# Kernel tuning notes

Measured on AMD Instinct MI355X. Metric: run time of the kernel, lower is better.

## Reference

```python
import jax, jax.numpy as jnp
import numpy as np

N, NH, D, REP, C, SUB = 512, 32, 1024, 1024, 16, 64
GAMA, EPS, LN_EPS = 0.9, 1e-10, 1e-5
IMG_H, IMG_W = 800, 1280


def spatial_enc(b1, b2, h, w):
    # pocket.ops.compute_spatial_encodings: 18 handcrafted pair features + their logs -> 36
    c1x = (b1[:, 0] + b1[:, 2]) * 0.5; c1y = (b1[:, 1] + b1[:, 3]) * 0.5
    c2x = (b2[:, 0] + b2[:, 2]) * 0.5; c2y = (b2[:, 1] + b2[:, 3]) * 0.5
    b1w = b1[:, 2] - b1[:, 0]; b1h = b1[:, 3] - b1[:, 1]
    b2w = b2[:, 2] - b2[:, 0]; b2h = b2[:, 3] - b2[:, 1]
    dx = jnp.abs(c2x - c1x) / (b1w + EPS)
    dy = jnp.abs(c2y - c1y) / (b1h + EPS)
    ltx = jnp.maximum(b1[:, 0], b2[:, 0]); lty = jnp.maximum(b1[:, 1], b2[:, 1])
    rbx = jnp.minimum(b1[:, 2], b2[:, 2]); rby = jnp.minimum(b1[:, 3], b2[:, 3])
    inter = jnp.clip(rbx - ltx, 0.0) * jnp.clip(rby - lty, 0.0)
    a1 = b1w * b1h; a2 = b2w * b2h
    iou = inter / (a1 + a2 - inter)
    f = jnp.stack([
        c1x / w, c1y / h, c2x / w, c2y / h,
        b1w / w, b1h / h, b2w / w, b2h / h,
        a1 / (h * w), a2 / (h * w), a2 / (a1 + EPS),
        b1w / (b1h + EPS), b2w / (b2h + EPS), iou,
        (c2x > c1x) * dx, (c2x < c1x) * dx,
        (c2y > c1y) * dy, (c2y < c1y) * dy,
    ], axis=1)
    return jnp.concatenate([f, jnp.log(f + EPS)], axis=1)


def mbf(a, s, w1, b1, w2, b2, w3, b3):
    # relu(sum_c fc3_c(relu(fc1_c(a) * fc2_c(s)))) with branches batched over c
    u1 = jnp.einsum('pd,cdk->cpk', a, w1) + b1[:, None, :]
    u2 = jnp.einsum('ps,csk->cpk', s, w2) + b2[:, None, :]
    hdn = jax.nn.relu(u1 * u2)  # [C,P,SUB]
    out = jnp.einsum('cpk,cko->po', hdn, w3) + b3.sum(0)
    return jax.nn.relu(out)


def ln(x, g, b):
    m = x.mean(-1, keepdims=True)
    v = ((x - m) ** 2).mean(-1, keepdims=True)
    return (x - m) / jnp.sqrt(v + LN_EPS) * g + b


def setup_inputs():
    key = jax.random.key(0)
    ks = jax.random.split(key, 16)
    labels = jnp.where(jnp.arange(N) < NH, 0, 1).astype(jnp.int32)  # first NH nodes are humans
    node = jax.random.normal(ks[0], (N, D), jnp.float32)
    cx = jax.random.uniform(ks[1], (N,)) * (IMG_W * 0.5)
    cy = jax.random.uniform(ks[2], (N,)) * (IMG_H * 0.5)
    bw = jax.random.uniform(ks[3], (N,)) * (IMG_W * 0.3) + 8.0
    bh = jax.random.uniform(ks[4], (N,)) * (IMG_H * 0.3) + 8.0
    coords = jnp.stack([cx, cy, cx + bw, cy + bh], axis=1)
    p = lambda k, shp: jax.random.normal(k, shp, jnp.float32) * 0.02
    return dict(
        labels=labels, node=node, coords=coords, image_h=IMG_H, image_w=IMG_W,
        sp_w1=p(ks[5], (36, 128)), sp_b1=jnp.zeros(128),
        sp_w2=p(ks[6], (128, 256)), sp_b2=jnp.zeros(256),
        sp_w3=p(ks[7], (256, 1024)), sp_b3=jnp.zeros(1024),
        att_w1=p(ks[8], (C, 2 * D, SUB)), att_b1=jnp.zeros((C, SUB)),
        att_w2=p(ks[9], (C, 1024, SUB)), att_b2=jnp.zeros((C, SUB)),
        att_w3=p(ks[10], (C, SUB, REP)), att_b3=jnp.zeros((C, REP)),
        adj_w=p(ks[11], (REP,)), adj_b=jnp.zeros(()),
        lnh_g=jnp.ones(D), lnh_b=jnp.zeros(D),
        lno_g=jnp.ones(D), lno_b=jnp.zeros(D),
    )


def reference(labels, node, coords, image_h, image_w,
              sp_w1, sp_b1, sp_w2, sp_b2, sp_w3, sp_b3,
              att_w1, att_b1, att_w2, att_b2, att_w3, att_b3,
              adj_w, adj_b, lnh_g, lnh_b, lno_g, lno_b):
    n = node.shape[0]
    n_h = int((np.asarray(labels) == 0).sum())
    xi = np.repeat(np.arange(n_h), n)  # human index per pair
    yj = np.tile(np.arange(n), n_h)    # node index per pair
    keep = np.nonzero(xi != yj)[0]
    x = jnp.asarray(xi); y = jnp.asarray(yj)
    x_keep = jnp.asarray(xi[keep]); y_keep = jnp.asarray(yj[keep])

    f = spatial_enc(coords[x], coords[y], float(image_h), float(image_w))  # [P,36]
    sp = jax.nn.relu(f @ sp_w1 + sp_b1)
    sp = jax.nn.relu(sp @ sp_w2 + sp_b2)
    sp = jax.nn.relu(sp @ sp_w3 + sp_b3)  # [P,1024]

    human_node = node[:n_h]
    adjacency = None
    for _ in range(2):  # num_iter
        a = jnp.concatenate([human_node[x], node[y]], axis=1)  # [P,2D]
        weight = mbf(a, sp, att_w1, att_b1, att_w2, att_b2, att_w3, att_b3)  # [P,REP]
        adjacency = jax.nn.relu(weight @ adj_w + adj_b).reshape(n_h, n)
        hn_msg = adjacency @ node          # einsum('yx,xa->ya', adj, node)
        nd_msg = adjacency.T @ human_node  # einsum('yx,xa->ya', adj.T, human)
        node = ln(node * GAMA + (1.0 - GAMA) * nd_msg, lno_g, lno_b)
        human_node = ln(human_node * GAMA + (1.0 - GAMA) * hn_msg, lnh_g, lnh_b)

    return (human_node[x_keep], node[y_keep], adjacency[x_keep, y_keep], x_keep, y_keep)
```

## Files before the change

kernel.cpp:

```cpp
#include <hip/hip_runtime.h>
#include <hip/hip_bf16.h>


typedef __attribute__((ext_vector_type(4))) float  f32x4;
typedef __attribute__((ext_vector_type(8))) __bf16 bf16x8;
typedef __attribute__((ext_vector_type(4))) __bf16 bf16x4;

#define FEPS 1e-10f
#define LNEPS 1e-5f
#define GAMA_F 0.9f

__device__ __forceinline__ void gload16(const void* g, void* l) {
  __builtin_amdgcn_global_load_lds(
      (const __attribute__((address_space(1))) void*)g,
      (__attribute__((address_space(3))) void*)l, 16, 0, 0);
}

__global__ void prep_all(const float* __restrict__ w1, const float* __restrict__ w2,
                         const float* __restrict__ w3, const float* __restrict__ spw3,
                         __bf16* __restrict__ W1at, __bf16* __restrict__ W1bt,
                         __bf16* __restrict__ W2t, __bf16* __restrict__ W3t,
                         __bf16* __restrict__ SpW3t) {
  __shared__ float tile[64][65];
  const int b = blockIdx.x, t = threadIdx.x;
  const int tc = t & 63, tr = t >> 6;
  if (b < 256) {
    const int c = b >> 4, d0 = (b & 15) << 6;
    #pragma unroll
    for (int pass = 0; pass < 2; ++pass) {
      const float* src = w1 + (size_t)c * 131072 + (size_t)(d0 + pass * 1024) * 64;
      __bf16* dst = pass ? W1bt : W1at;
      if (pass) __syncthreads();
      #pragma unroll
      for (int q = 0; q < 16; ++q) {
        int dd = q * 4 + tr;
        tile[dd][tc] = src[dd * 64 + tc];
      }
      __syncthreads();
      #pragma unroll
      for (int q = 0; q < 16; ++q) {
        int kk = q * 4 + tr;
        dst[(size_t)(c * 64 + kk) * 1024 + d0 + tc] = (__bf16)tile[tc][kk];
      }
    }
  } else if (b < 512) {
    const int bb = b - 256, c = bb >> 4, s0 = (bb & 15) << 6;
    const float* src = w2 + (size_t)c * 65536 + (size_t)s0 * 64;
    #pragma unroll
    for (int q = 0; q < 16; ++q) {
      int ss = q * 4 + tr;
      tile[ss][tc] = src[ss * 64 + tc];
    }
    __syncthreads();
    #pragma unroll
    for (int q = 0; q < 16; ++q) {
      int kk = q * 4 + tr;
      W2t[(size_t)(c * 64 + kk) * 1024 + s0 + tc] = (__bf16)tile[tc][kk];
    }
  } else if (b < 768) {
    const int bb = b - 512, c = bb >> 4, o0 = (bb & 15) << 6;
    const float* src = w3 + (size_t)c * 65536;
    #pragma unroll
    for (int q = 0; q < 16; ++q) {
      int kk = q * 4 + tr;
      tile[kk][tc] = src[kk * 1024 + o0 + tc];
    }
    __syncthreads();
    #pragma unroll
    for (int q = 0; q < 16; ++q) {
      int oo = q * 4 + tr;
      W3t[(size_t)(o0 + oo) * 1024 + c * 64 + tc] = (__bf16)tile[tc][oo];
    }
  } else {
    const int bb = b - 768, o0 = (bb >> 2) << 6, k0 = (bb & 3) << 6;
    #pragma unroll
    for (int q = 0; q < 16; ++q) {
      int kk = q * 4 + tr;
      tile[kk][tc] = spw3[(size_t)(k0 + kk) * 1024 + o0 + tc];
    }
    __syncthreads();
    #pragma unroll
    for (int q = 0; q < 16; ++q) {
      int oo = q * 4 + tr;
      SpW3t[(size_t)(o0 + oo) * 256 + k0 + tc] = (__bf16)tile[tc][oo];
    }
  }
}

__global__ void prep_sp2(const float* __restrict__ w1, const float* __restrict__ w2,
                         const float* __restrict__ b3,
                         __bf16* __restrict__ W1t, __bf16* __restrict__ W2t,
                         float* __restrict__ b3s) {
  int gid = blockIdx.x * 256 + threadIdx.x;
  if (gid < 8192) {
    int n = gid >> 6, k = gid & 63;
    W1t[gid] = (k < 36) ? (__bf16)w1[k * 128 + n] : (__bf16)0.f;
  }
  {
    int n = gid >> 7, k = gid & 127;
    W2t[gid] = (__bf16)w2[k * 256 + n];
  }
  if (gid < 1024) {
    float s = 0.f;
    for (int cc = 0; cc < 16; ++cc) s += b3[cc * 1024 + gid];
    b3s[gid] = s;
  }
}

__global__ void init_nodes(const float* __restrict__ node_in, float* __restrict__ node_f,
                           __bf16* __restrict__ node_b, float* __restrict__ hn_f,
                           __bf16* __restrict__ hn_b) {
  int gid = blockIdx.x * 256 + threadIdx.x;
  float v = node_in[gid];
  node_f[gid] = v;
  node_b[gid] = (__bf16)v;
  if (gid < 32 * 1024) { hn_f[gid] = v; hn_b[gid] = (__bf16)v; }
}

__device__ __forceinline__ float read_dim(const void* p) {
  int iv = *(const int*)p;
  if (iv > 0 && iv < (1 << 20)) return (float)iv;
  return *(const float*)p;
}

__global__ void spatial_k(const float* __restrict__ coords, const void* __restrict__ imh,
                          const void* __restrict__ imw, __bf16* __restrict__ f36) {
  int p = blockIdx.x * 256 + threadIdx.x;
  int i = p >> 9, j = p & 511;
  float H = read_dim(imh), W = read_dim(imw);
  f32x4 b1 = ((const f32x4*)coords)[i];
  f32x4 b2 = ((const f32x4*)coords)[j];
  float c1x = (b1[0] + b1[2]) * 0.5f, c1y = (b1[1] + b1[3]) * 0.5f;
  float c2x = (b2[0] + b2[2]) * 0.5f, c2y = (b2[1] + b2[3]) * 0.5f;
  float b1w = b1[2] - b1[0], b1h = b1[3] - b1[1];
  float b2w = b2[2] - b2[0], b2h = b2[3] - b2[1];
  float dx = fabsf(c2x - c1x) / (b1w + FEPS);
  float dy = fabsf(c2y - c1y) / (b1h + FEPS);
  float ltx = fmaxf(b1[0], b2[0]), lty = fmaxf(b1[1], b2[1]);
  float rbx = fminf(b1[2], b2[2]), rby = fminf(b1[3], b2[3]);
  float inter = fmaxf(rbx - ltx, 0.f) * fmaxf(rby - lty, 0.f);
  float a1 = b1w * b1h, a2 = b2w * b2h;
  float iou = inter / (a1 + a2 - inter);
  float f[18];
  f[0] = c1x / W;  f[1] = c1y / H;  f[2] = c2x / W;  f[3] = c2y / H;
  f[4] = b1w / W;  f[5] = b1h / H;  f[6] = b2w / W;  f[7] = b2h / H;
  f[8] = a1 / (H * W); f[9] = a2 / (H * W); f[10] = a2 / (a1 + FEPS);
  f[11] = b1w / (b1h + FEPS); f[12] = b2w / (b2h + FEPS); f[13] = iou;
  f[14] = (c2x > c1x) ? dx : 0.f; f[15] = (c2x < c1x) ? dx : 0.f;
  f[16] = (c2y > c1y) ? dy : 0.f; f[17] = (c2y < c1y) ? dy : 0.f;
  __bf16 o[64];
  #pragma unroll
  for (int q = 0; q < 18; ++q) { o[q] = (__bf16)f[q]; o[18 + q] = (__bf16)logf(f[q] + FEPS); }
  #pragma unroll
  for (int q = 36; q < 64; ++q) o[q] = (__bf16)0.f;
  bf16x8* dst = (bf16x8*)(f36 + (size_t)p * 64);
  #pragma unroll
  for (int q = 0; q < 8; ++q) dst[q] = *(bf16x8*)&o[q * 8];
}

template <int EPI>
__global__ __launch_bounds__(256)
void gemm_bt(const __bf16* __restrict__ A, const __bf16* __restrict__ Bt,
             const float* __restrict__ bias, void* __restrict__ C,
             int M, int N, int K,
             const float* __restrict__ adjw = nullptr,
             float* __restrict__ adjpre = nullptr) {
  __shared__ __align__(16) __bf16 As[128 * 64];
  __shared__ __align__(16) __bf16 Bs[128 * 64];
  const int t = threadIdx.x;
  const int lane = t & 63, wv = t >> 6;
  const int wr = wv >> 1, wc = wv & 1;
  const int lr = lane & 15, lg = lane >> 4;
  const int lrow = lane >> 3, lcol = (lane & 7) << 3;
  const int m0 = blockIdx.x * 128, n0 = blockIdx.y * 128;

  f32x4 acc[4][4] = {};
  const int nkt = K >> 6;
  for (int kt = 0; kt < nkt; ++kt) {
    const int k0 = kt << 6;
    #pragma unroll
    for (int it = 0; it < 4; ++it) {
      const int rbase = wv * 32 + it * 8;
      gload16(A + (size_t)(m0 + rbase + lrow) * K + k0 + lcol, &As[rbase * 64]);
      gload16(Bt + (size_t)(n0 + rbase + lrow) * K + k0 + lcol, &Bs[rbase * 64]);
    }
    __syncthreads();
    #pragma unroll
    for (int ks = 0; ks < 2; ++ks) {
      bf16x8 af[4], bfr[4];
      #pragma unroll
      for (int mi = 0; mi < 4; ++mi)
        af[mi] = *(const bf16x8*)&As[(wr * 64 + mi * 16 + lr) * 64 + ks * 32 + lg * 8];
      #pragma unroll
      for (int ni = 0; ni < 4; ++ni)
        bfr[ni] = *(const bf16x8*)&Bs[(wc * 64 + ni * 16 + lr) * 64 + ks * 32 + lg * 8];
      #pragma unroll
      for (int mi = 0; mi < 4; ++mi)
        #pragma unroll
        for (int ni = 0; ni < 4; ++ni)
          acc[mi][ni] = __builtin_amdgcn_mfma_f32_16x16x32_bf16(af[mi], bfr[ni], acc[mi][ni], 0, 0, 0);
    }
    __syncthreads();
  }

  if constexpr (EPI == 4) {
    float b3v[4], awv[4];
    #pragma unroll
    for (int ni = 0; ni < 4; ++ni) {
      int Cc = n0 + wc * 64 + ni * 16 + lr;
      b3v[ni] = bias[Cc];
      awv[ni] = adjw[Cc];
    }
    #pragma unroll
    for (int mi = 0; mi < 4; ++mi) {
      #pragma unroll
      for (int r = 0; r < 4; ++r) {
        float s = 0.f;
        #pragma unroll
        for (int ni = 0; ni < 4; ++ni)
          s += fmaxf(acc[mi][ni][r] + b3v[ni], 0.f) * awv[ni];
        s += __shfl_xor(s, 1);
        s += __shfl_xor(s, 2);
        s += __shfl_xor(s, 4);
        s += __shfl_xor(s, 8);
        if (lr == 0)
          atomicAdd(&adjpre[m0 + wr * 64 + mi * 16 + lg * 4 + r], s);
      }
    }
  } else {
    #pragma unroll
    for (int mi = 0; mi < 4; ++mi) {
      #pragma unroll
      for (int r = 0; r < 4; ++r) {
        int R = m0 + wr * 64 + mi * 16 + lg * 4 + r;
        #pragma unroll
        for (int ni = 0; ni < 4; ++ni) {
          int Cc = n0 + wc * 64 + ni * 16 + lr;
          float v = acc[mi][ni][r];
          if constexpr (EPI == 0) {
            ((__bf16*)C)[(size_t)R * N + Cc] = (__bf16)fmaxf(v + bias[Cc], 0.f);
          } else if constexpr (EPI == 1) {
            ((__bf16*)C)[(size_t)R * N + Cc] = (__bf16)(v + bias[Cc]);
          } else if constexpr (EPI == 2) {
            ((float*)C)[(size_t)R * N + Cc] = v + bias[Cc];
          } else {
            ((float*)C)[(size_t)R * N + Cc] = v;
          }
        }
      }
    }
  }
}

__global__ __launch_bounds__(256)
void gemm_u1(const __bf16* __restrict__ hn_b, const __bf16* __restrict__ node_b,
             const __bf16* __restrict__ W1at, const __bf16* __restrict__ W1bt,
             const float* __restrict__ b1, float* __restrict__ H1, float* __restrict__ N1) {
  __shared__ __align__(16) __bf16 As[32 * 64];
  __shared__ __align__(16) __bf16 Bs[128 * 64];
  const int t = threadIdx.x;
  const int lane = t & 63, wv = t >> 6;
  const int wr = wv >> 1, wc = wv & 1;
  const int lr = lane & 15, lg = lane >> 4;
  const int lrow = lane >> 3, lcol = (lane & 7) << 3;
  const bool isH = (blockIdx.x == 0);
  const __bf16* Ap = isH ? hn_b : node_b + (size_t)(blockIdx.x - 1) * 32 * 1024;
  const __bf16* Bp = isH ? W1at : W1bt;
  const int n0 = blockIdx.y * 128;

  f32x4 acc[4] = {};
  for (int kt = 0; kt < 16; ++kt) {
    const int k0 = kt << 6;
    gload16(Ap + (size_t)(wv * 8 + lrow) * 1024 + k0 + lcol, &As[(wv * 8) * 64]);
    #pragma unroll
    for (int it = 0; it < 4; ++it) {
      const int rbase = wv * 32 + it * 8;
      gload16(Bp + (size_t)(n0 + rbase + lrow) * 1024 + k0 + lcol, &Bs[rbase * 64]);
    }
    __syncthreads();
    #pragma unroll
    for (int ks = 0; ks < 2; ++ks) {
      bf16x8 af = *(const bf16x8*)&As[(wr * 16 + lr) * 64 + ks * 32 + lg * 8];
      #pragma unroll
      for (int ni = 0; ni < 4; ++ni) {
        bf16x8 bfr = *(const bf16x8*)&Bs[(wc * 64 + ni * 16 + lr) * 64 + ks * 32 + lg * 8];
        acc[ni] = __builtin_amdgcn_mfma_f32_16x16x32_bf16(af, bfr, acc[ni], 0, 0, 0);
      }
    }
    __syncthreads();
  }
  #pragma unroll
  for (int ni = 0; ni < 4; ++ni) {
    #pragma unroll
    for (int r = 0; r < 4; ++r) {
      int R = wr * 16 + lg * 4 + r;
      int Cc = n0 + wc * 64 + ni * 16 + lr;
      float v = acc[ni][r];
      if (isH) H1[(size_t)R * 1024 + Cc] = v + b1[Cc];
      else     N1[((size_t)(blockIdx.x - 1) * 32 + R) * 1024 + Cc] = v;
    }
  }
}

__global__ void build_hdn(const __bf16* __restrict__ u2, const float* __restrict__ H1,
                          const float* __restrict__ N1, __bf16* __restrict__ hdn) {
  int gid = blockIdx.x * 256 + threadIdx.x;
  int p = gid >> 7, c8 = (gid & 127) << 3;
  int i = p >> 9, j = p & 511;
  bf16x8 u = *(const bf16x8*)(u2 + (size_t)p * 1024 + c8);
  const float* hp = H1 + (size_t)i * 1024 + c8;
  const float* np = N1 + (size_t)j * 1024 + c8;
  f32x4 h0 = *(const f32x4*)hp, h1 = *(const f32x4*)(hp + 4);
  f32x4 n0 = *(const f32x4*)np, n1 = *(const f32x4*)(np + 4);
  bf16x8 o;
  #pragma unroll
  for (int e = 0; e < 4; ++e) {
    o[e]     = (__bf16)fmaxf((h0[e] + n0[e]) * (float)u[e], 0.f);
    o[4 + e] = (__bf16)fmaxf((h1[e] + n1[e]) * (float)u[4 + e], 0.f);
  }
  *(bf16x8*)(hdn + (size_t)p * 1024 + c8) = o;
}

__global__ void msg_k(const float* __restrict__ adjpre, const float* __restrict__ adjb,
                      const float* __restrict__ node, const float* __restrict__ hn,
                      float* __restrict__ hn_msg, float* __restrict__ nd_msg) {
  int row = blockIdx.x, t = threadIdx.x;
  float ab = adjb[0];
  if (row < 32) {
    f32x4 acc = {0.f, 0.f, 0.f, 0.f};
    for (int j = 0; j < 512; ++j)
      acc += fmaxf(adjpre[row * 512 + j] + ab, 0.f) * ((const f32x4*)node)[j * 256 + t];
    ((f32x4*)hn_msg)[row * 256 + t] = acc;
  } else {
    int j = row - 32;
    f32x4 acc = {0.f, 0.f, 0.f, 0.f};
    for (int i = 0; i < 32; ++i)
      acc += fmaxf(adjpre[i * 512 + j] + ab, 0.f) * ((const f32x4*)hn)[i * 256 + t];
    ((f32x4*)nd_msg)[j * 256 + t] = acc;
  }
}

__global__ void ln_k(float* __restrict__ node_f, float* __restrict__ hn_f,
                     const float* __restrict__ nd_msg, const float* __restrict__ hn_msg,
                     const float* __restrict__ lno_g, const float* __restrict__ lno_b,
                     const float* __restrict__ lnh_g, const float* __restrict__ lnh_b,
                     __bf16* __restrict__ node_bb, __bf16* __restrict__ hn_bb) {
  __shared__ float sbuf[4];
  int row = blockIdx.x, t = threadIdx.x;
  bool isN = row < 512;
  int r = isN ? row : row - 512;
  float* X = (isN ? node_f : hn_f) + (size_t)r * 1024;
  const float* Mg = (isN ? nd_msg : hn_msg) + (size_t)r * 1024;
  const float* g = isN ? lno_g : lnh_g;
  const float* bb = isN ? lno_b : lnh_b;
  __bf16* Xb = (isN ? node_bb : hn_bb) + (size_t)r * 1024;

  f32x4 x = ((const f32x4*)X)[t];
  f32x4 m = ((const f32x4*)Mg)[t];
  f32x4 y;
  #pragma unroll
  for (int e = 0; e < 4; ++e) y[e] = x[e] * GAMA_F + (1.0f - GAMA_F) * m[e];
  float s = y[0] + y[1] + y[2] + y[3];
  #pragma unroll
  for (int mm = 32; mm >= 1; mm >>= 1) s += __shfl_xor(s, mm);
  if ((t & 63) == 0) sbuf[t >> 6] = s;
  __syncthreads();
  float mean = (sbuf[0] + sbuf[1] + sbuf[2] + sbuf[3]) * (1.0f / 1024.0f);
  __syncthreads();
  f32x4 d;
  #pragma unroll
  for (int e = 0; e < 4; ++e) d[e] = y[e] - mean;
  float sq = d[0] * d[0] + d[1] * d[1] + d[2] * d[2] + d[3] * d[3];
  #pragma unroll
  for (int mm = 32; mm >= 1; mm >>= 1) sq += __shfl_xor(sq, mm);
  if ((t & 63) == 0) sbuf[t >> 6] = sq;
  __syncthreads();
  float var = (sbuf[0] + sbuf[1] + sbuf[2] + sbuf[3]) * (1.0f / 1024.0f);
  float inv = rsqrtf(var + LNEPS);
  f32x4 gg = ((const f32x4*)g)[t];
  f32x4 bv = ((const f32x4*)bb)[t];
  f32x4 o;
  bf16x4 ob;
  #pragma unroll
  for (int e = 0; e < 4; ++e) { o[e] = d[e] * inv * gg[e] + bv[e]; ob[e] = (__bf16)o[e]; }
  ((f32x4*)X)[t] = o;
  *(bf16x4*)(Xb + t * 4) = ob;
}

__global__ void gather_k(const float* __restrict__ hn, const float* __restrict__ node,
                         const float* __restrict__ adjpre, const float* __restrict__ adjb,
                         float* __restrict__ out) {
  int p = blockIdx.x, t = threadIdx.x;
  int i = p >> 9, j = p & 511;
  if (i == j) return;
  int m = p - (p + 512) / 513;
  float* out0 = out;
  float* out1 = out + (size_t)16352 * 1024;
  float* out2 = out1 + (size_t)16352 * 1024;
  ((f32x4*)out0)[(size_t)m * 256 + t] = ((const f32x4*)hn)[i * 256 + t];
  ((f32x4*)out1)[(size_t)m * 256 + t] = ((const f32x4*)node)[j * 256 + t];
  if (t == 0) {
    out2[m] = fmaxf(adjpre[p] + adjb[0], 0.f);
    out2[16352 + m] = (float)i;
    out2[2 * 16352 + m] = (float)j;
  }
}

extern "C" void kernel_launch(void* const* d_in, const int* in_sizes, int n_in,
                              void* d_out, int out_size, void* d_ws, size_t ws_size,
                              hipStream_t stream) {
  const float* node_in = (const float*)d_in[1];
  const float* coords  = (const float*)d_in[2];
  const void*  imh     = d_in[3];
  const void*  imw     = d_in[4];
  const float* sp_w1 = (const float*)d_in[5];
  const float* sp_b1 = (const float*)d_in[6];
  const float* sp_w2 = (const float*)d_in[7];
  const float* sp_b2 = (const float*)d_in[8];
  const float* sp_w3 = (const float*)d_in[9];
  const float* sp_b3 = (const float*)d_in[10];
  const float* att_w1 = (const float*)d_in[11];
  const float* att_b1 = (const float*)d_in[12];
  const float* att_w2 = (const float*)d_in[13];
  const float* att_b2 = (const float*)d_in[14];
  const float* att_w3 = (const float*)d_in[15];
  const float* att_b3 = (const float*)d_in[16];
  const float* adj_w  = (const float*)d_in[17];
  const float* adj_b  = (const float*)d_in[18];
  const float* lnh_g  = (const float*)d_in[19];
  const float* lnh_b  = (const float*)d_in[20];
  const float* lno_g  = (const float*)d_in[21];
  const float* lno_b  = (const float*)d_in[22];

  char* w = (char*)d_ws;
  size_t off = 0;
  auto alloc = [&](size_t bytes) -> char* {
    char* p = w + off;
    off += (bytes + 255) & ~(size_t)255;
    return p;
  };
  __bf16* W1at  = (__bf16*)alloc((size_t)1024 * 1024 * 2);
  __bf16* W1bt  = (__bf16*)alloc((size_t)1024 * 1024 * 2);
  __bf16* W2t   = (__bf16*)alloc((size_t)1024 * 1024 * 2);
  __bf16* W3t   = (__bf16*)alloc((size_t)1024 * 1024 * 2);
  __bf16* SpW1t = (__bf16*)alloc(128 * 64 * 2);
  __bf16* SpW2t = (__bf16*)alloc(256 * 128 * 2);
  __bf16* SpW3t = (__bf16*)alloc(1024 * 256 * 2);
  float*  b3s   = (float*)alloc(1024 * 4);
  __bf16* f36   = (__bf16*)alloc((size_t)16384 * 64 * 2);
  __bf16* sp1   = (__bf16*)alloc((size_t)16384 * 128 * 2);
  __bf16* sp2   = (__bf16*)alloc((size_t)16384 * 256 * 2);
  __bf16* spb   = (__bf16*)alloc((size_t)16384 * 1024 * 2);
  __bf16* u2    = (__bf16*)alloc((size_t)16384 * 1024 * 2);
  float*  H1    = (float*)alloc((size_t)32 * 1024 * 4);
  float*  N1    = (float*)alloc((size_t)512 * 1024 * 4);
  float*  adjpre = (float*)alloc(16384 * 4);
  float*  node_f = (float*)alloc((size_t)512 * 1024 * 4);
  float*  hn_f   = (float*)alloc((size_t)32 * 1024 * 4);
  __bf16* node_b = (__bf16*)alloc((size_t)512 * 1024 * 2);
  __bf16* hn_b   = (__bf16*)alloc((size_t)32 * 1024 * 2);
  float*  hn_msgb = (float*)alloc((size_t)32 * 1024 * 4);
  float*  nd_msgb = (float*)alloc((size_t)512 * 1024 * 4);
  if (off > ws_size) return;

  prep_all<<<832, 256, 0, stream>>>(att_w1, att_w2, att_w3, sp_w3, W1at, W1bt, W2t, W3t, SpW3t);
  prep_sp2<<<128, 256, 0, stream>>>(sp_w1, sp_w2, att_b3, SpW1t, SpW2t, b3s);
  init_nodes<<<2048, 256, 0, stream>>>(node_in, node_f, node_b, hn_f, hn_b);
  spatial_k<<<64, 256, 0, stream>>>(coords, imh, imw, f36);

  gemm_bt<0><<<dim3(128, 1), 256, 0, stream>>>(f36, SpW1t, sp_b1, sp1, 16384, 128, 64);
  gemm_bt<0><<<dim3(128, 2), 256, 0, stream>>>(sp1, SpW2t, sp_b2, sp2, 16384, 256, 128);
  gemm_bt<0><<<dim3(128, 8), 256, 0, stream>>>(sp2, SpW3t, sp_b3, spb, 16384, 1024, 256);
  gemm_bt<1><<<dim3(128, 8), 256, 0, stream>>>(spb, W2t, att_b2, u2, 16384, 1024, 1024);

  __bf16* hdn = spb;
  for (int iter = 0; iter < 2; ++iter) {
    gemm_u1<<<dim3(17, 8), 256, 0, stream>>>(hn_b, node_b, W1at, W1bt, att_b1, H1, N1);
    build_hdn<<<8192, 256, 0, stream>>>(u2, H1, N1, hdn);
    hipMemsetAsync(adjpre, 0, 16384 * 4, stream);
    gemm_bt<4><<<dim3(128, 8), 256, 0, stream>>>(hdn, W3t, b3s, nullptr, 16384, 1024, 1024,
                                                 adj_w, adjpre);
    msg_k<<<544, 256, 0, stream>>>(adjpre, adj_b, node_f, hn_f, hn_msgb, nd_msgb);
    ln_k<<<544, 256, 0, stream>>>(node_f, hn_f, nd_msgb, hn_msgb,
                                  lno_g, lno_b, lnh_g, lnh_b, node_b, hn_b);
  }

  gather_k<<<16384, 256, 0, stream>>>(hn_f, node_f, adjpre, adj_b, (float*)d_out);
}
```

Measured before the change: 525.6 us.

## Fuse prep kernels, MLP head, hdn build into GEMM, and msg+LN

Merges the four prep kernels into one launch and fuses the first two spatial MLP layers into a single kernel that keeps the intermediate in LDS. build_hdn is folded into the A-operand load of the W3 GEMM, which now splits N into four 256-wide slices and writes per-slice partial sums instead of using atomics and a memset. msg_k and ln_k are merged, with ping-pong node buffers. The aim is fewer launches and no 32MB hdn round trip, at the cost of recomputing the hdn elementwise per column slice and uncoalesced loads of u2 and N1 in the GEMM.

Measured after the change: 598.2 us. 13.8% more time.

```diff
diff --git a/kernel.cpp b/kernel.cpp
--- a/kernel.cpp
+++ b/kernel.cpp
@@ -16,11 +16,27 @@
       (__attribute__((address_space(3))) void*)l, 16, 0, 0);
 }
 
-__global__ void prep_all(const float* __restrict__ w1, const float* __restrict__ w2,
-                         const float* __restrict__ w3, const float* __restrict__ spw3,
-                         __bf16* __restrict__ W1at, __bf16* __restrict__ W1bt,
-                         __bf16* __restrict__ W2t, __bf16* __restrict__ W3t,
-                         __bf16* __restrict__ SpW3t) {
+__device__ __forceinline__ float read_dim(const void* p) {
+  int iv = *(const int*)p;
+  if (iv > 0 && iv < (1 << 20)) return (float)iv;
+  return *(const float*)p;
+}
+
+__global__ void prep_mega(const float* __restrict__ w1, const float* __restrict__ w2,
+                          const float* __restrict__ w3, const float* __restrict__ spw3,
+                          const float* __restrict__ spw1, const float* __restrict__ spw2,
+                          const float* __restrict__ b3,
+                          const float* __restrict__ node_in,
+                          const float* __restrict__ coords,
+                          const void* __restrict__ imh, const void* __restrict__ imw,
+                          __bf16* __restrict__ W1at, __bf16* __restrict__ W1bt,
+                          __bf16* __restrict__ W2t, __bf16* __restrict__ W3t,
+                          __bf16* __restrict__ SpW3t,
+                          __bf16* __restrict__ SpW1t, __bf16* __restrict__ SpW2t,
+                          float* __restrict__ b3s,
+                          float* __restrict__ node_f, __bf16* __restrict__ node_b,
+                          float* __restrict__ hn_f, __bf16* __restrict__ hn_b,
+                          __bf16* __restrict__ f36) {
   __shared__ float tile[64][65];
   const int b = blockIdx.x, t = threadIdx.x;
   const int tc = t & 63, tr = t >> 6;
@@ -71,7 +87,7 @@
       int oo = q * 4 + tr;
       W3t[(size_t)(o0 + oo) * 1024 + c * 64 + tc] = (__bf16)tile[tc][oo];
     }
-  } else {
+  } else if (b < 832) {
     const int bb = b - 768, o0 = (bb >> 2) << 6, k0 = (bb & 3) << 6;
     #pragma unroll
     for (int q = 0; q < 16; ++q) {
@@ -84,87 +100,154 @@
       int oo = q * 4 + tr;
       SpW3t[(size_t)(o0 + oo) * 256 + k0 + tc] = (__bf16)tile[tc][oo];
     }
-  }
-}
-
-__global__ void prep_sp2(const float* __restrict__ w1, const float* __restrict__ w2,
-                         const float* __restrict__ b3,
-                         __bf16* __restrict__ W1t, __bf16* __restrict__ W2t,
-                         float* __restrict__ b3s) {
-  int gid = blockIdx.x * 256 + threadIdx.x;
-  if (gid < 8192) {
-    int n = gid >> 6, k = gid & 63;
-    W1t[gid] = (k < 36) ? (__bf16)w1[k * 128 + n] : (__bf16)0.f;
-  }
+  } else if (b < 960) {
+    int gid = (b - 832) * 256 + t;
+    if (gid < 8192) {
+      int n = gid >> 6, k = gid & 63;
+      SpW1t[gid] = (k < 36) ? (__bf16)spw1[k * 128 + n] : (__bf16)0.f;
+    }
+    {
+      int n = gid >> 7, k = gid & 127;
+      SpW2t[gid] = (__bf16)spw2[k * 256 + n];
+    }
+    if (gid < 1024) {
+      float s = 0.f;
+      for (int cc = 0; cc < 16; ++cc) s += b3[cc * 1024 + gid];
+      b3s[gid] = s;
+    }
+  } else if (b < 3008) {
+    int gid = (b - 960) * 256 + t;
+    float v = node_in[gid];
+    node_f[gid] = v;
+    node_b[gid] = (__bf16)v;
+    if (gid < 32 * 1024) { hn_f[gid] = v; hn_b[gid] = (__bf16)v; }
+  } else {
+    int p = (b - 3008) * 256 + t;
+    int i = p >> 9, j = p & 511;
+    float H = read_dim(imh), W = read_dim(imw);
+    f32x4 b1 = ((const f32x4*)coords)[i];
+    f32x4 b2 = ((const f32x4*)coords)[j];
+    float c1x = (b1[0] + b1[2]) * 0.5f, c1y = (b1[1] + b1[3]) * 0.5f;
+    float c2x = (b2[0] + b2[2]) * 0.5f, c2y = (b2[1] + b2[3]) * 0.5f;
+    float b1w = b1[2] - b1[0], b1h = b1[3] - b1[1];
+    float b2w = b2[2] - b2[0], b2h = b2[3] - b2[1];
+    float dx = fabsf(c2x - c1x) / (b1w + FEPS);
+    float dy = fabsf(c2y - c1y) / (b1h + FEPS);
+    float ltx = fmaxf(b1[0], b2[0]), lty = fmaxf(b1[1], b2[1]);
+    float rbx = fminf(b1[2], b2[2]), rby = fminf(b1[3], b2[3]);
+    float inter = fmaxf(rbx - ltx, 0.f) * fmaxf(rby - lty, 0.f);
+    float a1 = b1w * b1h, a2 = b2w * b2h;
+    float iou = inter / (a1 + a2 - inter);
+    float f[18];
+    f[0] = c1x / W;  f[1] = c1y / H;  f[2] = c2x / W;  f[3] = c2y / H;
+    f[4] = b1w / W;  f[5] = b1h / H;  f[6] = b2w / W;  f[7] = b2h / H;
+    f[8] = a1 / (H * W); f[9] = a2 / (H * W); f[10] = a2 / (a1 + FEPS);
+    f[11] = b1w / (b1h + FEPS); f[12] = b2w / (b2h + FEPS); f[13] = iou;
+    f[14] = (c2x > c1x) ? dx : 0.f; f[15] = (c2x < c1x) ? dx : 0.f;
+    f[16] = (c2y > c1y) ? dy : 0.f; f[17] = (c2y < c1y) ? dy : 0.f;
+    __bf16 o[64];
+    #pragma unroll
+    for (int q = 0; q < 18; ++q) { o[q] = (__bf16)f[q]; o[18 + q] = (__bf16)logf(f[q] + FEPS); }
+    #pragma unroll
+    for (int q = 36; q < 64; ++q) o[q] = (__bf16)0.f;
+    bf16x8* dst = (bf16x8*)(f36 + (size_t)p * 64);
+    #pragma unroll
+    for (int q = 0; q < 8; ++q) dst[q] = *(bf16x8*)&o[q * 8];
+  }
+}
+
+__global__ __launch_bounds__(256)
+void mlp_head(const __bf16* __restrict__ f36, const __bf16* __restrict__ SpW1t,
+              const __bf16* __restrict__ SpW2t, const float* __restrict__ b1,
+              const float* __restrict__ b2, __bf16* __restrict__ sp2out) {
+  __shared__ __align__(16) __bf16 Af[128 * 64];
+  __shared__ __align__(16) __bf16 W1s[128 * 64];
+  __shared__ __align__(16) __bf16 S1[128 * 128];
+  __shared__ __align__(16) __bf16 W2s[256 * 128];
+  const int t = threadIdx.x;
+  const int lane = t & 63, wv = t >> 6;
+  const int wr = wv >> 1, wc = wv & 1;
+  const int lr = lane & 15, lg = lane >> 4;
+  const int m0 = blockIdx.x * 128;
+
+  #pragma unroll
+  for (int cc = 0; cc < 4; ++cc)
+    gload16(f36 + (size_t)m0 * 64 + (wv * 4 + cc) * 512 + lane * 8, &Af[(wv * 4 + cc) * 512 + lane * 8]);
+  #pragma unroll
+  for (int cc = 0; cc < 4; ++cc)
+    gload16(SpW1t + (wv * 4 + cc) * 512 + lane * 8, &W1s[(wv * 4 + cc) * 512 + lane * 8]);
+  #pragma unroll
+  for (int cc = 0; cc < 16; ++cc)
+    gload16(SpW2t + (wv * 16 + cc) * 512 + lane * 8, &W2s[(wv * 16 + cc) * 512 + lane * 8]);
+  __syncthreads();
+
   {
-    int n = gid >> 7, k = gid & 127;
-    W2t[gid] = (__bf16)w2[k * 256 + n];
-  }
-  if (gid < 1024) {
-    float s = 0.f;
-    for (int cc = 0; cc < 16; ++cc) s += b3[cc * 1024 + gid];
-    b3s[gid] = s;
-  }
-}
-
-__global__ void init_nodes(const float* __restrict__ node_in, float* __restrict__ node_f,
-                           __bf16* __restrict__ node_b, float* __restrict__ hn_f,
-                           __bf16* __restrict__ hn_b) {
-  int gid = blockIdx.x * 256 + threadIdx.x;
-  float v = node_in[gid];
-  node_f[gid] = v;
-  node_b[gid] = (__bf16)v;
-  if (gid < 32 * 1024) { hn_f[gid] = v; hn_b[gid] = (__bf16)v; }
-}
-
-__device__ __forceinline__ float read_dim(const void* p) {
-  int iv = *(const int*)p;
-  if (iv > 0 && iv < (1 << 20)) return (float)iv;
-  return *(const float*)p;
-}
-
-__global__ void spatial_k(const float* __restrict__ coords, const void* __restrict__ imh,
-                          const void* __restrict__ imw, __bf16* __restrict__ f36) {
-  int p = blockIdx.x * 256 + threadIdx.x;
-  int i = p >> 9, j = p & 511;
-  float H = read_dim(imh), W = read_dim(imw);
-  f32x4 b1 = ((const f32x4*)coords)[i];
-  f32x4 b2 = ((const f32x4*)coords)[j];
-  float c1x = (b1[0] + b1[2]) * 0.5f, c1y = (b1[1] + b1[3]) * 0.5f;
-  float c2x = (b2[0] + b2[2]) * 0.5f, c2y = (b2[1] + b2[3]) * 0.5f;
-  float b1w = b1[2] - b1[0], b1h = b1[3] - b1[1];
-  float b2w = b2[2] - b2[0], b2h = b2[3] - b2[1];
-  float dx = fabsf(c2x - c1x) / (b1w + FEPS);
-  float dy = fabsf(c2y - c1y) / (b1h + FEPS);
-  float ltx = fmaxf(b1[0], b2[0]), lty = fmaxf(b1[1], b2[1]);
-  float rbx = fminf(b1[2], b2[2]), rby = fminf(b1[3], b2[3]);
-  float inter = fmaxf(rbx - ltx, 0.f) * fmaxf(rby - lty, 0.f);
-  float a1 = b1w * b1h, a2 = b2w * b2h;
-  float iou = inter / (a1 + a2 - inter);
-  float f[18];
-  f[0] = c1x / W;  f[1] = c1y / H;  f[2] = c2x / W;  f[3] = c2y / H;
-  f[4] = b1w / W;  f[5] = b1h / H;  f[6] = b2w / W;  f[7] = b2h / H;
-  f[8] = a1 / (H * W); f[9] = a2 / (H * W); f[10] = a2 / (a1 + FEPS);
-  f[11] = b1w / (b1h + FEPS); f[12] = b2w / (b2h + FEPS); f[13] = iou;
-  f[14] = (c2x > c1x) ? dx : 0.f; f[15] = (c2x < c1x) ? dx : 0.f;
-  f[16] = (c2y > c1y) ? dy : 0.f; f[17] = (c2y < c1y) ? dy : 0.f;
-  __bf16 o[64];
-  #pragma unroll
-  for (int q = 0; q < 18; ++q) { o[q] = (__bf16)f[q]; o[18 + q] = (__bf16)logf(f[q] + FEPS); }
-  #pragma unroll
-  for (int q = 36; q < 64; ++q) o[q] = (__bf16)0.f;
-  bf16x8* dst = (bf16x8*)(f36 + (size_t)p * 64);
-  #pragma unroll
-  for (int q = 0; q < 8; ++q) dst[q] = *(bf16x8*)&o[q * 8];
+    f32x4 acc[4][4] = {};
+    #pragma unroll
+    for (int ks = 0; ks < 2; ++ks) {
+      bf16x8 af[4], bf[4];
+      #pragma unroll
+      for (int mi = 0; mi < 4; ++mi)
+        af[mi] = *(const bf16x8*)&Af[(wr * 64 + mi * 16 + lr) * 64 + ks * 32 + lg * 8];
+      #pragma unroll
+      for (int ni = 0; ni < 4; ++ni)
+        bf[ni] = *(const bf16x8*)&W1s[(wc * 64 + ni * 16 + lr) * 64 + ks * 32 + lg * 8];
+      #pragma unroll
+      for (int mi = 0; mi < 4; ++mi)
+        #pragma unroll
+        for (int ni = 0; ni < 4; ++ni)
+          acc[mi][ni] = __builtin_amdgcn_mfma_f32_16x16x32_bf16(af[mi], bf[ni], acc[mi][ni], 0, 0, 0);
+    }
+    __syncthreads();
+    #pragma unroll
+    for (int mi = 0; mi < 4; ++mi)
+      #pragma unroll
+      for (int r = 0; r < 4; ++r) {
+        int R = wr * 64 + mi * 16 + lg * 4 + r;
+        #pragma unroll
+        for (int ni = 0; ni < 4; ++ni) {
+          int Cc = wc * 64 + ni * 16 + lr;
+          S1[R * 128 + Cc] = (__bf16)fmaxf(acc[mi][ni][r] + b1[Cc], 0.f);
+        }
+      }
+  }
+  __syncthreads();
+
+  {
+    f32x4 acc[4][8] = {};
+    #pragma unroll
+    for (int ks = 0; ks < 4; ++ks) {
+      bf16x8 af[4];
+      #pragma unroll
+      for (int mi = 0; mi < 4; ++mi)
+        af[mi] = *(const bf16x8*)&S1[(wr * 64 + mi * 16 + lr) * 128 + ks * 32 + lg * 8];
+      #pragma unroll
+      for (int ni = 0; ni < 8; ++ni) {
+        bf16x8 bf = *(const bf16x8*)&W2s[(wc * 128 + ni * 16 + lr) * 128 + ks * 32 + lg * 8];
+        #pragma unroll
+        for (int mi = 0; mi < 4; ++mi)
+          acc[mi][ni] = __builtin_amdgcn_mfma_f32_16x16x32_bf16(af[mi], bf, acc[mi][ni], 0, 0, 0);
+      }
+    }
+    #pragma unroll
+    for (int mi = 0; mi < 4; ++mi)
+      #pragma unroll
+      for (int r = 0; r < 4; ++r) {
+        int R = m0 + wr * 64 + mi * 16 + lg * 4 + r;
+        #pragma unroll
+        for (int ni = 0; ni < 8; ++ni) {
+          int Cc = wc * 128 + ni * 16 + lr;
+          sp2out[(size_t)R * 256 + Cc] = (__bf16)fmaxf(acc[mi][ni][r] + b2[Cc], 0.f);
+        }
+      }
+  }
 }
 
 template <int EPI>
 __global__ __launch_bounds__(256)
 void gemm_bt(const __bf16* __restrict__ A, const __bf16* __restrict__ Bt,
              const float* __restrict__ bias, void* __restrict__ C,
-             int M, int N, int K,
-             const float* __restrict__ adjw = nullptr,
-             float* __restrict__ adjpre = nullptr) {
+             int M, int N, int K) {
   __shared__ __align__(16) __bf16 As[128 * 64];
   __shared__ __align__(16) __bf16 Bs[128 * 64];
   const int t = threadIdx.x;
@@ -202,54 +285,19 @@
     }
     __syncthreads();
   }
-
-  if constexpr (EPI == 4) {
-    float b3v[4], awv[4];
-    #pragma unroll
-    for (int ni = 0; ni < 4; ++ni) {
-      int Cc = n0 + wc * 64 + ni * 16 + lr;
-      b3v[ni] = bias[Cc];
-      awv[ni] = adjw[Cc];
-    }
-    #pragma unroll
-    for (int mi = 0; mi < 4; ++mi) {
-      #pragma unroll
-      for (int r = 0; r < 4; ++r) {
-        float s = 0.f;
-        #pragma unroll
-        for (int ni = 0; ni < 4; ++ni)
-          s += fmaxf(acc[mi][ni][r] + b3v[ni], 0.f) * awv[ni];
-        s += __shfl_xor(s, 1);
-        s += __shfl_xor(s, 2);
-        s += __shfl_xor(s, 4);
-        s += __shfl_xor(s, 8);
-        if (lr == 0)
-          atomicAdd(&adjpre[m0 + wr * 64 + mi * 16 + lg * 4 + r], s);
-      }
-    }
-  } else {
-    #pragma unroll
-    for (int mi = 0; mi < 4; ++mi) {
-      #pragma unroll
-      for (int r = 0; r < 4; ++r) {
-        int R = m0 + wr * 64 + mi * 16 + lg * 4 + r;
-        #pragma unroll
-        for (int ni = 0; ni < 4; ++ni) {
-          int Cc = n0 + wc * 64 + ni * 16 + lr;
-          float v = acc[mi][ni][r];
-          if constexpr (EPI == 0) {
-            ((__bf16*)C)[(size_t)R * N + Cc] = (__bf16)fmaxf(v + bias[Cc], 0.f);
-          } else if constexpr (EPI == 1) {
-            ((__bf16*)C)[(size_t)R * N + Cc] = (__bf16)(v + bias[Cc]);
-          } else if constexpr (EPI == 2) {
-            ((float*)C)[(size_t)R * N + Cc] = v + bias[Cc];
-          } else {
-            ((float*)C)[(size_t)R * N + Cc] = v;
-          }
-        }
-      }
-    }
-  }
+  #pragma unroll
+  for (int mi = 0; mi < 4; ++mi)
+    #pragma unroll
+    for (int r = 0; r < 4; ++r) {
+      int R = m0 + wr * 64 + mi * 16 + lg * 4 + r;
+      #pragma unroll
+      for (int ni = 0; ni < 4; ++ni) {
+        int Cc = n0 + wc * 64 + ni * 16 + lr;
+        float v = acc[mi][ni][r] + bias[Cc];
+        if constexpr (EPI == 0) v = fmaxf(v, 0.f);
+        ((__bf16*)C)[(size_t)R * N + Cc] = (__bf16)v;
+      }
+    }
 }
 
 __global__ __launch_bounds__(256)
@@ -290,7 +338,7 @@
     __syncthreads();
   }
   #pragma unroll
-  for (int ni = 0; ni < 4; ++ni) {
+  for (int ni = 0; ni < 4; ++ni)
     #pragma unroll
     for (int r = 0; r < 4; ++r) {
       int R = wr * 16 + lg * 4 + r;
@@ -299,67 +347,156 @@
       if (isH) H1[(size_t)R * 1024 + Cc] = v + b1[Cc];
       else     N1[((size_t)(blockIdx.x - 1) * 32 + R) * 1024 + Cc] = v;
     }
-  }
-}
-
-__global__ void build_hdn(const __bf16* __restrict__ u2, const float* __restrict__ H1,
-                          const float* __restrict__ N1, __bf16* __restrict__ hdn) {
-  int gid = blockIdx.x * 256 + threadIdx.x;
-  int p = gid >> 7, c8 = (gid & 127) << 3;
-  int i = p >> 9, j = p & 511;
-  bf16x8 u = *(const bf16x8*)(u2 + (size_t)p * 1024 + c8);
-  const float* hp = H1 + (size_t)i * 1024 + c8;
-  const float* np = N1 + (size_t)j * 1024 + c8;
-  f32x4 h0 = *(const f32x4*)hp, h1 = *(const f32x4*)(hp + 4);
-  f32x4 n0 = *(const f32x4*)np, n1 = *(const f32x4*)(np + 4);
-  bf16x8 o;
-  #pragma unroll
-  for (int e = 0; e < 4; ++e) {
-    o[e]     = (__bf16)fmaxf((h0[e] + n0[e]) * (float)u[e], 0.f);
-    o[4 + e] = (__bf16)fmaxf((h1[e] + n1[e]) * (float)u[4 + e], 0.f);
-  }
-  *(bf16x8*)(hdn + (size_t)p * 1024 + c8) = o;
-}
-
-__global__ void msg_k(const float* __restrict__ adjpre, const float* __restrict__ adjb,
-                      const float* __restrict__ node, const float* __restrict__ hn,
-                      float* __restrict__ hn_msg, float* __restrict__ nd_msg) {
-  int row = blockIdx.x, t = threadIdx.x;
-  float ab = adjb[0];
-  if (row < 32) {
-    f32x4 acc = {0.f, 0.f, 0.f, 0.f};
-    for (int j = 0; j < 512; ++j)
-      acc += fmaxf(adjpre[row * 512 + j] + ab, 0.f) * ((const f32x4*)node)[j * 256 + t];
-    ((f32x4*)hn_msg)[row * 256 + t] = acc;
+}
+
+__global__ __launch_bounds__(256, 2)
+void adj_fused(const __bf16* __restrict__ u2, const float* __restrict__ H1,
+               const float* __restrict__ N1, const __bf16* __restrict__ W3t,
+               const float* __restrict__ b3s, const float* __restrict__ adjw,
+               float* __restrict__ adjpre4) {
+  __shared__ __align__(16) __bf16 Bs[256 * 64];
+  __shared__ float redbuf[2][128];
+  const int t = threadIdx.x;
+  const int lane = t & 63, wv = t >> 6;
+  const int wr = wv >> 1, wc = wv & 1;
+  const int lr = lane & 15, lg = lane >> 4;
+  const int lrow = lane >> 3, lcol = (lane & 7) << 3;
+  const int m0 = blockIdx.x * 128;
+  const int h = blockIdx.y;
+  const int c0 = h * 256;
+  const int i_h = m0 >> 9;
+  const int j0 = m0 & 511;
+
+  f32x4 acc[2][4][4] = {};
+  for (int kt = 0; kt < 16; ++kt) {
+    const int k0 = kt << 6;
+    #pragma unroll
+    for (int it = 0; it < 8; ++it) {
+      const int rbase = wv * 64 + it * 8;
+      gload16(W3t + (size_t)(c0 + rbase + lrow) * 1024 + k0 + lcol, &Bs[rbase * 64]);
+    }
+    float hk[2][8];
+    #pragma unroll
+    for (int ks = 0; ks < 2; ++ks) {
+      const float* hp = H1 + (size_t)i_h * 1024 + k0 + ks * 32 + lg * 8;
+      f32x4 a0 = *(const f32x4*)hp;
+      f32x4 a1 = *(const f32x4*)(hp + 4);
+      #pragma unroll
+      for (int e = 0; e < 4; ++e) { hk[ks][e] = a0[e]; hk[ks][4 + e] = a1[e]; }
+    }
+    bf16x8 af[4][2];
+    #pragma unroll
+    for (int mi = 0; mi < 4; ++mi) {
+      const int ro = wr * 64 + mi * 16 + lr;
+      const __bf16* up = u2 + (size_t)(m0 + ro) * 1024 + k0;
+      const float* np = N1 + (size_t)(j0 + ro) * 1024 + k0;
+      #pragma unroll
+      for (int ks = 0; ks < 2; ++ks) {
+        bf16x8 u = *(const bf16x8*)(up + ks * 32 + lg * 8);
+        f32x4 n0v = *(const f32x4*)(np + ks * 32 + lg * 8);
+        f32x4 n1v = *(const f32x4*)(np + ks * 32 + lg * 8 + 4);
+        bf16x8 o;
+        #pragma unroll
+        for (int e = 0; e < 4; ++e) {
+          o[e]     = (__bf16)fmaxf((hk[ks][e] + n0v[e]) * (float)u[e], 0.f);
+          o[4 + e] = (__bf16)fmaxf((hk[ks][4 + e] + n1v[e]) * (float)u[4 + e], 0.f);
+        }
+        af[mi][ks] = o;
+      }
+    }
+    __syncthreads();
+    #pragma unroll
+    for (int nt = 0; nt < 2; ++nt)
+      #pragma unroll
+      for (int ks = 0; ks < 2; ++ks) {
+        bf16x8 bfr[4];
+        #pragma unroll
+        for (int ni = 0; ni < 4; ++ni)
+          bfr[ni] = *(const bf16x8*)&Bs[(nt * 128 + wc * 64 + ni * 16 + lr) * 64 + ks * 32 + lg * 8];
+        #pragma unroll
+        for (int mi = 0; mi < 4; ++mi)
+          #pragma unroll
+          for (int ni = 0; ni < 4; ++ni)
+            acc[nt][mi][ni] = __builtin_amdgcn_mfma_f32_16x16x32_bf16(af[mi][ks], bfr[ni], acc[nt][mi][ni], 0, 0, 0);
+      }
+    __syncthreads();
+  }
+
+  float b3v[2][4], awv[2][4];
+  #pragma unroll
+  for (int nt = 0; nt < 2; ++nt)
+    #pragma unroll
+    for (int ni = 0; ni < 4; ++ni) {
+      int Cc = c0 + nt * 128 + wc * 64 + ni * 16 + lr;
+      b3v[nt][ni] = b3s[Cc];
+      awv[nt][ni] = adjw[Cc];
+    }
+  #pragma unroll
+  for (int mi = 0; mi < 4; ++mi)
+    #pragma unroll
+    for (int r = 0; r < 4; ++r) {
+      float s = 0.f;
+      #pragma unroll
+      for (int nt = 0; nt < 2; ++nt)
+        #pragma unroll
+        for (int ni = 0; ni < 4; ++ni)
+          s += fmaxf(acc[nt][mi][ni][r] + b3v[nt][ni], 0.f) * awv[nt][ni];
+      s += __shfl_xor(s, 1);
+      s += __shfl_xor(s, 2);
+      s += __shfl_xor(s, 4);
+      s += __shfl_xor(s, 8);
+      if (lr == 0)
+        redbuf[wc][wr * 64 + mi * 16 + lg * 4 + r] = s;
+    }
+  __syncthreads();
+  if (t < 128)
+    adjpre4[(size_t)h * 16384 + m0 + t] = redbuf[0][t] + redbuf[1][t];
+}
+
+__global__ void msgln(const float* __restrict__ adjpre4, const float* __restrict__ adjb,
+                      const float* __restrict__ node_in_f, const float* __restrict__ hn_in_f,
+                      const float* __restrict__ lno_g, const float* __restrict__ lno_b,
+                      const float* __restrict__ lnh_g, const float* __restrict__ lnh_b,
+                      float* __restrict__ node_out_f, float* __restrict__ hn_out_f,
+                      __bf16* __restrict__ node_bb, __bf16* __restrict__ hn_bb) {
+  __shared__ float sbuf[4];
+  const int row = blockIdx.x, t = threadIdx.x;
+  const float ab = adjb[0];
+  const bool isH = row < 32;
+  f32x4 msg = {0.f, 0.f, 0.f, 0.f};
+  if (isH) {
+    const int i = row;
+    for (int j = 0; j < 512; j += 4) {
+      f32x4 a0 = *(const f32x4*)(adjpre4 + i * 512 + j);
+      f32x4 a1 = *(const f32x4*)(adjpre4 + 16384 + i * 512 + j);
+      f32x4 a2 = *(const f32x4*)(adjpre4 + 32768 + i * 512 + j);
+      f32x4 a3 = *(const f32x4*)(adjpre4 + 49152 + i * 512 + j);
+      #pragma unroll
+      for (int e = 0; e < 4; ++e) {
+        float a = fmaxf(a0[e] + a1[e] + a2[e] + a3[e] + ab, 0.f);
+        msg += a * ((const f32x4*)node_in_f)[(j + e) * 256 + t];
+      }
+    }
   } else {
-    int j = row - 32;
-    f32x4 acc = {0.f, 0.f, 0.f, 0.f};
-    for (int i = 0; i < 32; ++i)
-      acc += fmaxf(adjpre[i * 512 + j] + ab, 0.f) * ((const f32x4*)hn)[i * 256 + t];
-    ((f32x4*)nd_msg)[j * 256 + t] = acc;
-  }
-}
-
-__global__ void ln_k(float* __restrict__ node_f, float* __restrict__ hn_f,
-                     const float* __restrict__ nd_msg, const float* __restrict__ hn_msg,
-                     const float* __restrict__ lno_g, const float* __restrict__ lno_b,
-                     const float* __restrict__ lnh_g, const float* __restrict__ lnh_b,
-                     __bf16* __restrict__ node_bb, __bf16* __restrict__ hn_bb) {
-  __shared__ float sbuf[4];
-  int row = blockIdx.x, t = threadIdx.x;
-  bool isN = row < 512;
-  int r = isN ? row : row - 512;
-  float* X = (isN ? node_f : hn_f) + (size_t)r * 1024;
-  const float* Mg = (isN ? nd_msg : hn_msg) + (size_t)r * 1024;
-  const float* g = isN ? lno_g : lnh_g;
-  const float* bb = isN ? lno_b : lnh_b;
-  __bf16* Xb = (isN ? node_bb : hn_bb) + (size_t)r * 1024;
+    const int j = row - 32;
+    for (int i = 0; i < 32; ++i) {
+      int p = i * 512 + j;
+      float a = fmaxf(adjpre4[p] + adjpre4[16384 + p] + adjpre4[32768 + p] +
+                      adjpre4[49152 + p] + ab, 0.f);
+      msg += a * ((const f32x4*)hn_in_f)[i * 256 + t];
+    }
+  }
+  const int r = isH ? row : row - 32;
+  const float* X = (isH ? hn_in_f : node_in_f) + (size_t)r * 1024;
+  const float* g = isH ? lnh_g : lno_g;
+  const float* bb = isH ? lnh_b : lno_b;
+  float* Xo = (isH ? hn_out_f : node_out_f) + (size_t)r * 1024;
+  __bf16* Xb = (isH ? hn_bb : node_bb) + (size_t)r * 1024;
 
   f32x4 x = ((const f32x4*)X)[t];
-  f32x4 m = ((const f32x4*)Mg)[t];
   f32x4 y;
   #pragma unroll
-  for (int e = 0; e < 4; ++e) y[e] = x[e] * GAMA_F + (1.0f - GAMA_F) * m[e];
+  for (int e = 0; e < 4; ++e) y[e] = x[e] * GAMA_F + (1.0f - GAMA_F) * msg[e];
   float s = y[0] + y[1] + y[2] + y[3];
   #pragma unroll
   for (int mm = 32; mm >= 1; mm >>= 1) s += __shfl_xor(s, mm);
@@ -383,12 +520,12 @@
   bf16x4 ob;
   #pragma unroll
   for (int e = 0; e < 4; ++e) { o[e] = d[e] * inv * gg[e] + bv[e]; ob[e] = (__bf16)o[e]; }
-  ((f32x4*)X)[t] = o;
+  ((f32x4*)Xo)[t] = o;
   *(bf16x4*)(Xb + t * 4) = ob;
 }
 
 __global__ void gather_k(const float* __restrict__ hn, const float* __restrict__ node,
-                         const float* __restrict__ adjpre, const float* __restrict__ adjb,
+                         const float* __restrict__ adjpre4, const float* __restrict__ adjb,
                          float* __restrict__ out) {
   int p = blockIdx.x, t = threadIdx.x;
   int i = p >> 9, j = p & 511;
@@ -400,7 +537,8 @@
   ((f32x4*)out0)[(size_t)m * 256 + t] = ((const f32x4*)hn)[i * 256 + t];
   ((f32x4*)out1)[(size_t)m * 256 + t] = ((const f32x4*)node)[j * 256 + t];
   if (t == 0) {
-    out2[m] = fmaxf(adjpre[p] + adjb[0], 0.f);
+    out2[m] = fmaxf(adjpre4[p] + adjpre4[16384 + p] + adjpre4[32768 + p] +
+                    adjpre4[49152 + p] + adjb[0], 0.f);
     out2[16352 + m] = (float)i;
     out2[2 * 16352 + m] = (float)j;
   }
@@ -448,42 +586,38 @@
   __bf16* SpW3t = (__bf16*)alloc(1024 * 256 * 2);
   float*  b3s   = (float*)alloc(1024 * 4);
   __bf16* f36   = (__bf16*)alloc((size_t)16384 * 64 * 2);
-  __bf16* sp1   = (__bf16*)alloc((size_t)16384 * 128 * 2);
   __bf16* sp2   = (__bf16*)alloc((size_t)16384 * 256 * 2);
   __bf16* spb   = (__bf16*)alloc((size_t)16384 * 1024 * 2);
   __bf16* u2    = (__bf16*)alloc((size_t)16384 * 1024 * 2);
   float*  H1    = (float*)alloc((size_t)32 * 1024 * 4);
   float*  N1    = (float*)alloc((size_t)512 * 1024 * 4);
-  float*  adjpre = (float*)alloc(16384 * 4);
-  float*  node_f = (float*)alloc((size_t)512 * 1024 * 4);
-  float*  hn_f   = (float*)alloc((size_t)32 * 1024 * 4);
-  __bf16* node_b = (__bf16*)alloc((size_t)512 * 1024 * 2);
-  __bf16* hn_b   = (__bf16*)alloc((size_t)32 * 1024 * 2);
-  float*  hn_msgb = (float*)alloc((size_t)32 * 1024 * 4);
-  float*  nd_msgb = (float*)alloc((size_t)512 * 1024 * 4);
+  float*  adjpre4 = (float*)alloc((size_t)4 * 16384 * 4);
+  float*  node_f0 = (float*)alloc((size_t)512 * 1024 * 4);
+  float*  node_f1 = (float*)alloc((size_t)512 * 1024 * 4);
+  float*  hn_f0   = (float*)alloc((size_t)32 * 1024 * 4);
+  float*  hn_f1   = (float*)alloc((size_t)32 * 1024 * 4);
+  __bf16* node_b  = (__bf16*)alloc((size_t)512 * 1024 * 2);
+  __bf16* hn_b    = (__bf16*)alloc((size_t)32 * 1024 * 2);
   if (off > ws_size) return;
 
-  prep_all<<<832, 256, 0, stream>>>(att_w1, att_w2, att_w3, sp_w3, W1at, W1bt, W2t, W3t, SpW3t);
-  prep_sp2<<<128, 256, 0, stream>>>(sp_w1, sp_w2, att_b3, SpW1t, SpW2t, b3s);
-  init_nodes<<<2048, 256, 0, stream>>>(node_in, node_f, node_b, hn_f, hn_b);
-  spatial_k<<<64, 256, 0, stream>>>(coords, imh, imw, f36);
-
-  gemm_bt<0><<<dim3(128, 1), 256, 0, stream>>>(f36, SpW1t, sp_b1, sp1, 16384, 128, 64);
-  gemm_bt<0><<<dim3(128, 2), 256, 0, stream>>>(sp1, SpW2t, sp_b2, sp2, 16384, 256, 128);
+  prep_mega<<<3072, 256, 0, stream>>>(att_w1, att_w2, att_w3, sp_w3, sp_w1, sp_w2, att_b3,
+                                      node_in, coords, imh, imw,
+                                      W1at, W1bt, W2t, W3t, SpW3t, SpW1t, SpW2t, b3s,
+                                      node_f0, node_b, hn_f0, hn_b, f36);
+  mlp_head<<<128, 256, 0, stream>>>(f36, SpW1t, SpW2t, sp_b1, sp_b2, sp2);
   gemm_bt<0><<<dim3(128, 8), 256, 0, stream>>>(sp2, SpW3t, sp_b3, spb, 16384, 1024, 256);
   gemm_bt<1><<<dim3(128, 8), 256, 0, stream>>>(spb, W2t, att_b2, u2, 16384, 1024, 1024);
 
-  __bf16* hdn = spb;
-  for (int iter = 0; iter < 2; ++iter) {
-    gemm_u1<<<dim3(17, 8), 256, 0, stream>>>(hn_b, node_b, W1at, W1bt, att_b1, H1, N1);
-    build_hdn<<<8192, 256, 0, stream>>>(u2, H1, N1, hdn);
-    hipMemsetAsync(adjpre, 0, 16384 * 4, stream);
-    gemm_bt<4><<<dim3(128, 8), 256, 0, stream>>>(hdn, W3t, b3s, nullptr, 16384, 1024, 1024,
-                                                 adj_w, adjpre);
-    msg_k<<<544, 256, 0, stream>>>(adjpre, adj_b, node_f, hn_f, hn_msgb, nd_msgb);
-    ln_k<<<544, 256, 0, stream>>>(node_f, hn_f, nd_msgb, hn_msgb,
-                                  lno_g, lno_b, lnh_g, lnh_b, node_b, hn_b);
-  }
-
-  gather_k<<<16384, 256, 0, stream>>>(hn_f, node_f, adjpre, adj_b, (float*)d_out);
-}
+  gemm_u1<<<dim3(17, 8), 256, 0, stream>>>(hn_b, node_b, W1at, W1bt, att_b1, H1, N1);
+  adj_fused<<<dim3(128, 4), 256, 0, stream>>>(u2, H1, N1, W3t, b3s, adj_w, adjpre4);
+  msgln<<<544, 256, 0, stream>>>(adjpre4, adj_b, node_f0, hn_f0,
+                                 lno_g, lno_b, lnh_g, lnh_b,
+                                 node_f1, hn_f1, node_b, hn_b);
+  gemm_u1<<<dim3(17, 8), 256, 0, stream>>>(hn_b, node_b, W1at, W1bt, att_b1, H1, N1);
+  adj_fused<<<dim3(128, 4), 256, 0, stream>>>(u2, H1, N1, W3t, b3s, adj_w, adjpre4);
+  msgln<<<544, 256, 0, stream>>>(adjpre4, adj_b, node_f1, hn_f1,
+                                 lno_g, lno_b, lnh_g, lnh_b,
+                                 node_f0, hn_f0, node_b, hn_b);
+
+  gather_k<<<16384, 256, 0, stream>>>(hn_f0, node_f0, adjpre4, adj_b, (float*)d_out);
+}
```
